# Optimization experiments

Measured on AMD Instinct MI355X. Metric: run time of the kernel, lower is better.

Reference implementation:

```python
import jax, jax.numpy as jnp
import numpy as np

B, C, H, W = 4, 64, 128, 128
D_INNER, D_STATE, DT_RANK, K = 192, 16, 6, 4  # d_model = 3*C//2 = 96, expand = 2
EPS = 1e-5


def _haar():
    # pywt db1: dec_lo=[s,s], dec_hi=[-s,s]; code reverses dec_* and uses rec_* in
    # original order -> for Haar both dec and rec filter banks are identical.
    s = np.float32(1.0 / np.sqrt(2.0))
    lo = np.array([s, s], np.float32)
    hi = np.array([s, -s], np.float32)
    # stack order: [lo(i)lo(j), hi(i)lo(j), lo(i)hi(j), hi(i)hi(j)]
    return np.stack([np.outer(lo, lo), np.outer(hi, lo),
                     np.outer(lo, hi), np.outer(hi, hi)], 0)  # (4,2,2)

DEC = jnp.asarray(_haar())
REC = jnp.asarray(_haar())
DN = ('NCHW', 'OIHW', 'NCHW')


def _ln(x, s, b):
    m = x.mean(-1, keepdims=True)
    v = x.var(-1, keepdims=True)
    return (x - m) * jax.lax.rsqrt(v + EPS) * s + b


def _wt(x):
    b, c, h, w = x.shape
    wf = jnp.tile(DEC[:, None], (c, 1, 1, 1))  # (4c,1,2,2), groups=c, pad=0 for db1
    y = jax.lax.conv_general_dilated(x, wf, (2, 2), 'VALID',
                                     feature_group_count=c, dimension_numbers=DN)
    return y.reshape(b, c, 4, h // 2, w // 2)


def _iwt(x):
    # conv_transpose2d(stride=2, pad=0, groups=c) == lhs-dilated conv with flipped kernel, pad k-1
    b, c = x.shape[0], x.shape[1]
    h2, w2 = x.shape[3], x.shape[4]
    xr = x.reshape(b, c * 4, h2, w2)
    wf = jnp.tile(REC[:, ::-1, ::-1][None], (c, 1, 1, 1))  # (c,4,2,2)
    return jax.lax.conv_general_dilated(xr, wf, (1, 1), ((1, 1), (1, 1)),
                                        lhs_dilation=(2, 2), feature_group_count=c,
                                        dimension_numbers=DN)


def _ss2d(x, in_proj_w, conv_dw_w, conv_dw_b, x_proj_w, dt_proj_w, dt_proj_b,
          A_log, Ds, out_norm_s, out_norm_b, out_proj_w):
    b, d, h, w = x.shape  # d == D_INNER
    L = h * w
    xz = jnp.einsum('bchw,ec->behw', x, in_proj_w)  # (b,2d,h,w)
    x1, z = xz[:, :d], xz[:, d:]
    x1 = jax.lax.conv_general_dilated(x1, conv_dw_w, (1, 1), ((1, 1), (1, 1)),
                                      feature_group_count=d, dimension_numbers=DN)
    x1 = jax.nn.silu(x1 + conv_dw_b[None, :, None, None])
    # 4-direction flattening: hw, wh, and their reverses
    xf = x1.reshape(b, d, L)
    xt = x1.transpose(0, 1, 3, 2).reshape(b, d, L)
    xs = jnp.stack([xf, xt], 1)
    xs = jnp.concatenate([xs, xs[..., ::-1]], 1)  # (b,K,d,L)
    x_dbl = jnp.einsum('bkdl,kcd->bkcl', xs, x_proj_w)
    dts = x_dbl[:, :, :DT_RANK]
    Bs = x_dbl[:, :, DT_RANK:DT_RANK + D_STATE]   # (b,K,n,L)
    Cs = x_dbl[:, :, DT_RANK + D_STATE:]
    delta = jax.nn.softplus(jnp.einsum('bkrl,kdr->bkdl', dts, dt_proj_w)
                            + dt_proj_b[None, :, :, None])
    A = -jnp.exp(A_log)  # (K,d,n)

    def step(hc, inp):
        d_t, u_t, b_t, c_t = inp  # (b,K,d),(b,K,d),(b,K,n),(b,K,n)
        dA = jnp.exp(d_t[..., None] * A[None])
        hc = hc * dA + (d_t * u_t)[..., None] * b_t[:, :, None, :]
        y = jnp.einsum('bkdn,bkn->bkd', hc, c_t)
        return hc, y

    h0 = jnp.zeros((b, K, d, D_STATE), x.dtype)
    inputs = (delta.transpose(3, 0, 1, 2), xs.transpose(3, 0, 1, 2),
              Bs.transpose(3, 0, 1, 2), Cs.transpose(3, 0, 1, 2))
    _, ys = jax.lax.scan(step, h0, inputs)            # (L,b,K,d)
    out_y = ys.transpose(1, 2, 3, 0) + xs * Ds[None, :, :, None]  # (b,K,d,L)
    inv_y = out_y[:, 2:][..., ::-1]
    wh = out_y[:, 1].reshape(b, d, w, h).transpose(0, 1, 3, 2).reshape(b, d, L)
    invwh = inv_y[:, 1].reshape(b, d, w, h).transpose(0, 1, 3, 2).reshape(b, d, L)
    y = out_y[:, 0] + inv_y[:, 0] + wh + invwh        # (b,d,L)
    y = _ln(y.reshape(b, d, h, w).transpose(0, 2, 3, 1), out_norm_s, out_norm_b)
    y = y * jax.nn.silu(z.transpose(0, 2, 3, 1))
    y = jnp.einsum('bhwd,ed->bhwe', y, out_proj_w)
    return y.transpose(0, 3, 1, 2)


def reference(x, wt_low_scale, wt_high_scale, low_conv_w, in_proj_w, conv_dw_w,
              conv_dw_b, x_proj_w, dt_proj_w, dt_proj_b, A_log, Ds,
              out_norm_s, out_norm_b, out_proj_w, ln2_s, ln2_b, eca_w):
    b, c = x.shape[0], x.shape[1]
    wt = _wt(x)                                       # (b,c,4,h2,w2)
    h2, w2 = wt.shape[3], wt.shape[4]
    low = wt[:, :, 0] * wt_low_scale
    high = wt[:, :, 1:].reshape(b, c * 3, h2, w2) * wt_high_scale
    low = jax.nn.silu(jnp.einsum('bchw,ec->behw', low, low_conv_w[:, :, 0, 0]))
    high = _ss2d(high, in_proj_w, conv_dw_w, conv_dw_b, x_proj_w, dt_proj_w,
                 dt_proj_b, A_log, Ds, out_norm_s, out_norm_b, out_proj_w)
    high = _ln(high.transpose(0, 2, 3, 1), ln2_s, ln2_b).transpose(0, 3, 1, 2)
    mamba = jnp.tile(low, (1, 3, 1, 1)) * high
    merged = jnp.concatenate([low, mamba], 1).reshape(b, c, 4, h2, w2)
    y = _iwt(merged)                                  # (b,c,h,w)
    # ECA: gap -> conv1d(k=5) over channels -> sigmoid gate
    pooled = y.mean((2, 3))[:, None, :]               # (b,1,c)
    att = jax.lax.conv_general_dilated(pooled, eca_w.reshape(1, 1, 5), (1,),
                                       ((2, 2),), dimension_numbers=('NCH', 'OIH', 'NCH'))
    att = jax.nn.sigmoid(att[:, 0])
    return y * att[:, :, None, None] + x


def setup_inputs():
    key = jax.random.key(0)
    ks = jax.random.split(key, 20)
    f = jax.random.normal
    return {
        'x': f(ks[0], (B, C, H, W), jnp.float32),
        'wt_low_scale': jax.random.uniform(ks[1], (1, C, 1, 1), jnp.float32),
        'wt_high_scale': jax.random.uniform(ks[2], (1, 3 * C, 1, 1), jnp.float32),
        'low_conv_w': f(ks[3], (C, C, 1, 1), jnp.float32) * 0.1,
        'in_proj_w': f(ks[4], (2 * D_INNER, D_INNER), jnp.float32) * 0.05,
        'conv_dw_w': f(ks[5], (D_INNER, 1, 3, 3), jnp.float32) * 0.3,
        'conv_dw_b': f(ks[6], (D_INNER,), jnp.float32) * 0.1,
        'x_proj_w': f(ks[7], (K, DT_RANK + 2 * D_STATE, D_INNER), jnp.float32) * 0.05,
        'dt_proj_w': f(ks[8], (K, D_INNER, DT_RANK), jnp.float32) * 0.1,
        'dt_proj_b': jax.random.uniform(ks[9], (K, D_INNER), jnp.float32) - 4.0,
        'A_log': jax.random.uniform(ks[10], (K, D_INNER, D_STATE), jnp.float32),
        'Ds': f(ks[11], (K, D_INNER), jnp.float32) * 0.1,
        'out_norm_s': jnp.ones((D_INNER,), jnp.float32),
        'out_norm_b': jnp.zeros((D_INNER,), jnp.float32),
        'out_proj_w': f(ks[12], (D_INNER, D_INNER), jnp.float32) * 0.05,
        'ln2_s': jnp.ones((3 * C,), jnp.float32),
        'ln2_b': jnp.zeros((3 * C,), jnp.float32),
        'eca_w': f(ks[13], (5,), jnp.float32) * 0.3,
    }
```

## Files before the change

kernel.cpp:

```cpp
#include <hip/hip_runtime.h>

constexpr int cB = 4, cC = 64, cH = 128, cW = 128;
constexpr int cL = 4096;
constexpr int cD = 192, cN = 16;
constexpr int NCH = 64, CHUNK = 64;

__device__ __forceinline__ float silu_f(float v) { return v / (1.f + __expf(-v)); }

__global__ __launch_bounds__(256) void k_wt(const float* __restrict__ x,
                                            const float* __restrict__ wls,
                                            const float* __restrict__ whs,
                                            float* __restrict__ lraw,
                                            float* __restrict__ high) {
    int idx = blockIdx.x * 256 + threadIdx.x;
    int j = idx & 63, i = (idx >> 6) & 63, c = (idx >> 12) & 63, b = idx >> 18;
    const float* xp = x + (((size_t)(b * cC + c)) * cH + 2 * i) * cW + 2 * j;
    float x00 = xp[0], x01 = xp[1], x10 = xp[cW], x11 = xp[cW + 1];
    float s0 = 0.5f * (x00 + x01 + x10 + x11);
    float s1 = 0.5f * (x00 + x01 - x10 - x11);
    float s2 = 0.5f * (x00 - x01 + x10 - x11);
    float s3 = 0.5f * (x00 - x01 - x10 + x11);
    int l = i * 64 + j;
    lraw[(size_t)(b * cC + c) * cL + l] = s0 * wls[c];
    int ch = c * 3;
    high[(size_t)(b * cD + ch + 0) * cL + l] = s1 * whs[ch + 0];
    high[(size_t)(b * cD + ch + 1) * cL + l] = s2 * whs[ch + 1];
    high[(size_t)(b * cD + ch + 2) * cL + l] = s3 * whs[ch + 2];
}

__global__ __launch_bounds__(256) void k_lowconv(const float* __restrict__ lraw,
                                                 const float* __restrict__ w,
                                                 float* __restrict__ lowT) {
    int bid = blockIdx.x;
    int lt0 = (bid & 63) * 64;
    int b = bid >> 6;
    __shared__ float sW[16][68];
    __shared__ float sI[16][68];
    int tid = threadIdx.x;
    int tl = tid & 15, te = tid >> 4;
    float acc[4][4];
#pragma unroll
    for (int i = 0; i < 4; i++)
#pragma unroll
        for (int j = 0; j < 4; j++) acc[i][j] = 0.f;
    for (int c0 = 0; c0 < 64; c0 += 16) {
#pragma unroll
        for (int q = 0; q < 4; q++) {
            int tt = tid + q * 256;
            int cc = tt & 15, ee = tt >> 4;
            sW[cc][ee] = w[ee * 64 + c0 + cc];
        }
#pragma unroll
        for (int q = 0; q < 4; q++) {
            int tt = tid + q * 256;
            int ll = tt & 63, cc = tt >> 6;
            sI[cc][ll] = lraw[(size_t)(b * cC + c0 + cc) * cL + lt0 + ll];
        }
        __syncthreads();
#pragma unroll
        for (int cc = 0; cc < 16; cc++) {
            float4 wv = *reinterpret_cast<const float4*>(&sW[cc][te * 4]);
            float4 iv = *reinterpret_cast<const float4*>(&sI[cc][tl * 4]);
            acc[0][0] = fmaf(wv.x, iv.x, acc[0][0]); acc[0][1] = fmaf(wv.x, iv.y, acc[0][1]);
            acc[0][2] = fmaf(wv.x, iv.z, acc[0][2]); acc[0][3] = fmaf(wv.x, iv.w, acc[0][3]);
            acc[1][0] = fmaf(wv.y, iv.x, acc[1][0]); acc[1][1] = fmaf(wv.y, iv.y, acc[1][1]);
            acc[1][2] = fmaf(wv.y, iv.z, acc[1][2]); acc[1][3] = fmaf(wv.y, iv.w, acc[1][3]);
            acc[2][0] = fmaf(wv.z, iv.x, acc[2][0]); acc[2][1] = fmaf(wv.z, iv.y, acc[2][1]);
            acc[2][2] = fmaf(wv.z, iv.z, acc[2][2]); acc[2][3] = fmaf(wv.z, iv.w, acc[2][3]);
            acc[3][0] = fmaf(wv.w, iv.x, acc[3][0]); acc[3][1] = fmaf(wv.w, iv.y, acc[3][1]);
            acc[3][2] = fmaf(wv.w, iv.z, acc[3][2]); acc[3][3] = fmaf(wv.w, iv.w, acc[3][3]);
        }
        __syncthreads();
    }
    int ebase = te * 4;
    int lbase = lt0 + tl * 4;
#pragma unroll
    for (int j = 0; j < 4; j++) {
        float4 v = make_float4(silu_f(acc[0][j]), silu_f(acc[1][j]), silu_f(acc[2][j]), silu_f(acc[3][j]));
        *reinterpret_cast<float4*>(&lowT[((size_t)b * cL + lbase + j) * 64 + ebase]) = v;
    }
}

__global__ __launch_bounds__(256) void k_inproj(const float* __restrict__ hi,
                                                const float* __restrict__ w,
                                                float* __restrict__ xout,
                                                float* __restrict__ zT) {
    int bid = blockIdx.x;
    int et = bid % 6;
    int blt = bid / 6;
    int lt0 = (blt & 63) * 64;
    int b = blt >> 6;
    int e0 = et * 64;
    __shared__ float sW[16][68];
    __shared__ float sI[16][68];
    int tid = threadIdx.x;
    int tl = tid & 15, te = tid >> 4;
    float acc[4][4];
#pragma unroll
    for (int i = 0; i < 4; i++)
#pragma unroll
        for (int j = 0; j < 4; j++) acc[i][j] = 0.f;
    for (int c0 = 0; c0 < 192; c0 += 16) {
#pragma unroll
        for (int q = 0; q < 4; q++) {
            int tt = tid + q * 256;
            int cc = tt & 15, ee = tt >> 4;
            sW[cc][ee] = w[(e0 + ee) * 192 + c0 + cc];
        }
#pragma unroll
        for (int q = 0; q < 4; q++) {
            int tt = tid + q * 256;
            int ll = tt & 63, cc = tt >> 6;
            sI[cc][ll] = hi[(size_t)(b * cD + c0 + cc) * cL + lt0 + ll];
        }
        __syncthreads();
#pragma unroll
        for (int cc = 0; cc < 16; cc++) {
            float4 wv = *reinterpret_cast<const float4*>(&sW[cc][te * 4]);
            float4 iv = *reinterpret_cast<const float4*>(&sI[cc][tl * 4]);
            acc[0][0] = fmaf(wv.x, iv.x, acc[0][0]); acc[0][1] = fmaf(wv.x, iv.y, acc[0][1]);
            acc[0][2] = fmaf(wv.x, iv.z, acc[0][2]); acc[0][3] = fmaf(wv.x, iv.w, acc[0][3]);
            acc[1][0] = fmaf(wv.y, iv.x, acc[1][0]); acc[1][1] = fmaf(wv.y, iv.y, acc[1][1]);
            acc[1][2] = fmaf(wv.y, iv.z, acc[1][2]); acc[1][3] = fmaf(wv.y, iv.w, acc[1][3]);
            acc[2][0] = fmaf(wv.z, iv.x, acc[2][0]); acc[2][1] = fmaf(wv.z, iv.y, acc[2][1]);
            acc[2][2] = fmaf(wv.z, iv.z, acc[2][2]); acc[2][3] = fmaf(wv.z, iv.w, acc[2][3]);
            acc[3][0] = fmaf(wv.w, iv.x, acc[3][0]); acc[3][1] = fmaf(wv.w, iv.y, acc[3][1]);
            acc[3][2] = fmaf(wv.w, iv.z, acc[3][2]); acc[3][3] = fmaf(wv.w, iv.w, acc[3][3]);
        }
        __syncthreads();
    }
    int ebase = e0 + te * 4;
    int lbase = lt0 + tl * 4;
    if (ebase < 192) {
#pragma unroll
        for (int i = 0; i < 4; i++) {
            *reinterpret_cast<float4*>(&xout[(size_t)(b * cD + ebase + i) * cL + lbase]) =
                make_float4(acc[i][0], acc[i][1], acc[i][2], acc[i][3]);
        }
    } else {
#pragma unroll
        for (int j = 0; j < 4; j++) {
            *reinterpret_cast<float4*>(&zT[((size_t)b * cL + lbase + j) * 192 + (ebase - 192)]) =
                make_float4(acc[0][j], acc[1][j], acc[2][j], acc[3][j]);
        }
    }
}

__global__ __launch_bounds__(256) void k_dwconv(const float* __restrict__ xin,
                                                const float* __restrict__ w,
                                                const float* __restrict__ bias,
                                                float* __restrict__ x1,
                                                float* __restrict__ u1) {
    int bd = blockIdx.x;
    int d = bd % cD;
    const float* xp = xin + (size_t)bd * cL;
    float wv[9];
#pragma unroll
    for (int t = 0; t < 9; t++) wv[t] = w[d * 9 + t];
    float bv = bias[d];
    __shared__ float sm[64][65];
    int tid = threadIdx.x;
#pragma unroll
    for (int q = 0; q < 16; q++) {
        int p = tid + q * 256;
        int i = p >> 6, j = p & 63;
        float acc = bv;
#pragma unroll
        for (int di = 0; di < 3; di++) {
            int ii = i + di - 1;
            if (ii < 0 || ii >= 64) continue;
#pragma unroll
            for (int dj = 0; dj < 3; dj++) {
                int jj = j + dj - 1;
                if (jj < 0 || jj >= 64) continue;
                acc = fmaf(wv[di * 3 + dj], xp[ii * 64 + jj], acc);
            }
        }
        sm[i][j] = silu_f(acc);
    }
    __syncthreads();
#pragma unroll
    for (int q = 0; q < 16; q++) {
        int p = tid + q * 256;
        x1[(size_t)bd * cL + p] = sm[p >> 6][p & 63];
        u1[(size_t)bd * cL + p] = sm[p & 63][p >> 6];
    }
}

__global__ __launch_bounds__(256) void k_xproj(const float* __restrict__ x1,
                                               const float* __restrict__ u1,
                                               const float* __restrict__ xpw,
                                               float* __restrict__ xdbl) {
    int bid = blockIdx.x;
    int lt0 = (bid & 63) * 64;
    int k = (bid >> 6) & 3;
    int b = bid >> 8;
    const float* src = (k & 1) ? u1 : x1;
    bool rev = (k >= 2);
    __shared__ float sW[16][68];
    __shared__ float sI[16][68];
    int tid = threadIdx.x;
    int tl = tid & 15, te = tid >> 4;
    float acc[4][4];
#pragma unroll
    for (int i = 0; i < 4; i++)
#pragma unroll
        for (int j = 0; j < 4; j++) acc[i][j] = 0.f;
    for (int c0 = 0; c0 < 192; c0 += 16) {
#pragma unroll
        for (int q = 0; q < 4; q++) {
            int tt = tid + q * 256;
            int cc = tt & 15, ee = tt >> 4;
            sW[cc][ee] = (ee < 38) ? xpw[(k * 38 + ee) * 192 + c0 + cc] : 0.f;
        }
#pragma unroll
        for (int q = 0; q < 4; q++) {
            int tt = tid + q * 256;
            int ll = tt & 63, cc = tt >> 6;
            int l = lt0 + ll;
            int lm = rev ? (cL - 1 - l) : l;
            sI[cc][ll] = src[(size_t)(b * cD + c0 + cc) * cL + lm];
        }
        __syncthreads();
#pragma unroll
        for (int cc = 0; cc < 16; cc++) {
            float4 wv = *reinterpret_cast<const float4*>(&sW[cc][te * 4]);
            float4 iv = *reinterpret_cast<const float4*>(&sI[cc][tl * 4]);
            acc[0][0] = fmaf(wv.x, iv.x, acc[0][0]); acc[0][1] = fmaf(wv.x, iv.y, acc[0][1]);
            acc[0][2] = fmaf(wv.x, iv.z, acc[0][2]); acc[0][3] = fmaf(wv.x, iv.w, acc[0][3]);
            acc[1][0] = fmaf(wv.y, iv.x, acc[1][0]); acc[1][1] = fmaf(wv.y, iv.y, acc[1][1]);
            acc[1][2] = fmaf(wv.y, iv.z, acc[1][2]); acc[1][3] = fmaf(wv.y, iv.w, acc[1][3]);
            acc[2][0] = fmaf(wv.z, iv.x, acc[2][0]); acc[2][1] = fmaf(wv.z, iv.y, acc[2][1]);
            acc[2][2] = fmaf(wv.z, iv.z, acc[2][2]); acc[2][3] = fmaf(wv.z, iv.w, acc[2][3]);
            acc[3][0] = fmaf(wv.w, iv.x, acc[3][0]); acc[3][1] = fmaf(wv.w, iv.y, acc[3][1]);
            acc[3][2] = fmaf(wv.w, iv.z, acc[3][2]); acc[3][3] = fmaf(wv.w, iv.w, acc[3][3]);
        }
        __syncthreads();
    }
    int lbase = lt0 + tl * 4;
#pragma unroll
    for (int i = 0; i < 4; i++) {
        int e = te * 4 + i;
        if (e < 38) {
            *reinterpret_cast<float4*>(&xdbl[(size_t)((b * 4 + k) * 38 + e) * cL + lbase]) =
                make_float4(acc[i][0], acc[i][1], acc[i][2], acc[i][3]);
        }
    }
}

__global__ __launch_bounds__(192) void k_scan1(const float* __restrict__ xdbl,
                                               const float* __restrict__ x1,
                                               const float* __restrict__ u1,
                                               const float* __restrict__ dtw,
                                               const float* __restrict__ dtb,
                                               const float* __restrict__ alog,
                                               float* __restrict__ P,
                                               float* __restrict__ S) {
    int bid = blockIdx.x;
    int ch = bid % NCH;
    int bk = bid / NCH;
    int k = bk & 3, b = bk >> 2;
    int tid = threadIdx.x;
    int d = tid;
    float Av2[16], h[16];
#pragma unroll
    for (int j = 0; j < 16; j++) {
        Av2[j] = -__expf(alog[(k * 192 + d) * 16 + j]) * 1.44269504088896f;
        h[j] = 0.f;
    }
    float dtbv = dtb[k * 192 + d];
    float dtwv[6];
#pragma unroll
    for (int r = 0; r < 6; r++) dtwv[r] = dtw[(k * 192 + d) * 6 + r];
    const float* dtrows = xdbl + (size_t)(bk * 38) * cL;
    const float* Brow = xdbl + (size_t)(bk * 38 + 6) * cL;
    const float* ubase = ((k & 1) ? u1 : x1) + ((size_t)b * cD + d) * cL;
    bool rev = (k >= 2);

    __shared__ float sB[2][16][16];
    __shared__ float sdt[2][16][8];

    int rowA = tid >> 4, colA = tid & 15;
    int p0 = ch * CHUNK;

    for (int idx = tid; idx < 256; idx += 192)
        sB[0][idx & 15][idx >> 4] = Brow[(size_t)(idx >> 4) * cL + p0 + (idx & 15)];
    if (tid < 96) sdt[0][colA][rowA] = dtrows[(size_t)rowA * cL + p0 + colA];

    float Q = 0.f;
    int cur = 0;
    for (int t0 = p0; t0 < p0 + CHUNK; t0 += 16) {
        __syncthreads();
        if (t0 + 16 < p0 + CHUNK) {
            int t1 = t0 + 16;
            for (int idx = tid; idx < 256; idx += 192)
                sB[cur ^ 1][idx & 15][idx >> 4] = Brow[(size_t)(idx >> 4) * cL + t1 + (idx & 15)];
            if (tid < 96) sdt[cur ^ 1][colA][rowA] = dtrows[(size_t)rowA * cL + t1 + colA];
        }
        float uvals[16];
        {
            const float* up = rev ? (ubase + (cL - 16 - t0)) : (ubase + t0);
#pragma unroll
            for (int q = 0; q < 4; q++)
                *reinterpret_cast<float4*>(&uvals[q * 4]) = *reinterpret_cast<const float4*>(up + q * 4);
        }
#pragma unroll
        for (int l = 0; l < 16; l++) {
            float acc = dtbv;
#pragma unroll
            for (int r = 0; r < 6; r++) acc = fmaf(dtwv[r], sdt[cur][l][r], acc);
            float sp = fmaxf(acc, 0.f) + __logf(1.f + __expf(-fabsf(acc)));
            Q += sp;
            float uv = rev ? uvals[15 - l] : uvals[l];
            float duB = sp * uv;
            float Bv[16];
            *reinterpret_cast<float4*>(&Bv[0])  = *reinterpret_cast<const float4*>(&sB[cur][l][0]);
            *reinterpret_cast<float4*>(&Bv[4])  = *reinterpret_cast<const float4*>(&sB[cur][l][4]);
            *reinterpret_cast<float4*>(&Bv[8])  = *reinterpret_cast<const float4*>(&sB[cur][l][8]);
            *reinterpret_cast<float4*>(&Bv[12]) = *reinterpret_cast<const float4*>(&sB[cur][l][12]);
#pragma unroll
            for (int j = 0; j < 16; j++)
                h[j] = fmaf(h[j], exp2f(sp * Av2[j]), duB * Bv[j]);
        }
        cur ^= 1;
    }
    size_t base = (size_t)bid * 16 * 192 + d;
#pragma unroll
    for (int j = 0; j < 16; j++) {
        P[base + (size_t)j * 192] = exp2f(Av2[j] * Q);
        S[base + (size_t)j * 192] = h[j];
    }
}

__global__ __launch_bounds__(256) void k_carry(const float* __restrict__ P,
                                               float* __restrict__ S) {
    int gid = blockIdx.x * 256 + threadIdx.x;
    int d = gid % 192;
    int n = (gid / 192) & 15;
    int bk = gid / 3072;
    float h = 0.f;
    for (int c = 0; c < NCH; c++) {
        size_t idx = ((size_t)(bk * NCH + c) * 16 + n) * 192 + d;
        h = fmaf(P[idx], h, S[idx]);
        S[idx] = h;
    }
}

__global__ __launch_bounds__(192) void k_scan2(const float* __restrict__ xdbl,
                                               const float* __restrict__ x1,
                                               const float* __restrict__ u1,
                                               const float* __restrict__ dtw,
                                               const float* __restrict__ dtb,
                                               const float* __restrict__ alog,
                                               const float* __restrict__ dss,
                                               const float* __restrict__ S,
                                               float* __restrict__ yacc) {
    int bid = blockIdx.x;
    int ch = bid % NCH;
    int bk = bid / NCH;
    int k = bk & 3, b = bk >> 2;
    int tid = threadIdx.x;
    int d = tid;
    float Av2[16], h[16];
#pragma unroll
    for (int j = 0; j < 16; j++) {
        Av2[j] = -__expf(alog[(k * 192 + d) * 16 + j]) * 1.44269504088896f;
        h[j] = (ch == 0) ? 0.f : S[((size_t)(bk * NCH + ch - 1) * 16 + j) * 192 + d];
    }
    float Dv = dss[k * 192 + d];
    float dtbv = dtb[k * 192 + d];
    float dtwv[6];
#pragma unroll
    for (int r = 0; r < 6; r++) dtwv[r] = dtw[(k * 192 + d) * 6 + r];
    const float* dtrows = xdbl + (size_t)(bk * 38) * cL;
    const float* Brow = xdbl + (size_t)(bk * 38 + 6) * cL;
    const float* Crow = xdbl + (size_t)(bk * 38 + 22) * cL;
    const float* ubase = ((k & 1) ? u1 : x1) + ((size_t)b * cD + d) * cL;
    bool rev = (k >= 2);

    __shared__ float sB[2][16][16];
    __shared__ float sC[2][16][16];
    __shared__ float sdt[2][16][8];

    int rowA = tid >> 4, colA = tid & 15;
    int p0 = ch * CHUNK;

    for (int idx = tid; idx < 256; idx += 192) {
        sB[0][idx & 15][idx >> 4] = Brow[(size_t)(idx >> 4) * cL + p0 + (idx & 15)];
        sC[0][idx & 15][idx >> 4] = Crow[(size_t)(idx >> 4) * cL + p0 + (idx & 15)];
    }
    if (tid < 96) sdt[0][colA][rowA] = dtrows[(size_t)rowA * cL + p0 + colA];

    int cur = 0;
    for (int t0 = p0; t0 < p0 + CHUNK; t0 += 16) {
        __syncthreads();
        if (t0 + 16 < p0 + CHUNK) {
            int t1 = t0 + 16;
            for (int idx = tid; idx < 256; idx += 192) {
                sB[cur ^ 1][idx & 15][idx >> 4] = Brow[(size_t)(idx >> 4) * cL + t1 + (idx & 15)];
                sC[cur ^ 1][idx & 15][idx >> 4] = Crow[(size_t)(idx >> 4) * cL + t1 + (idx & 15)];
            }
            if (tid < 96) sdt[cur ^ 1][colA][rowA] = dtrows[(size_t)rowA * cL + t1 + colA];
        }
        float uvals[16];
        {
            const float* up = rev ? (ubase + (cL - 16 - t0)) : (ubase + t0);
#pragma unroll
            for (int q = 0; q < 4; q++)
                *reinterpret_cast<float4*>(&uvals[q * 4]) = *reinterpret_cast<const float4*>(up + q * 4);
        }
#pragma unroll
        for (int l = 0; l < 16; l++) {
            float acc = dtbv;
#pragma unroll
            for (int r = 0; r < 6; r++) acc = fmaf(dtwv[r], sdt[cur][l][r], acc);
            float sp = fmaxf(acc, 0.f) + __logf(1.f + __expf(-fabsf(acc)));
            float uv = rev ? uvals[15 - l] : uvals[l];
            float duB = sp * uv;
            float Bv[16], Cv[16];
            *reinterpret_cast<float4*>(&Bv[0])  = *reinterpret_cast<const float4*>(&sB[cur][l][0]);
            *reinterpret_cast<float4*>(&Bv[4])  = *reinterpret_cast<const float4*>(&sB[cur][l][4]);
            *reinterpret_cast<float4*>(&Bv[8])  = *reinterpret_cast<const float4*>(&sB[cur][l][8]);
            *reinterpret_cast<float4*>(&Bv[12]) = *reinterpret_cast<const float4*>(&sB[cur][l][12]);
            *reinterpret_cast<float4*>(&Cv[0])  = *reinterpret_cast<const float4*>(&sC[cur][l][0]);
            *reinterpret_cast<float4*>(&Cv[4])  = *reinterpret_cast<const float4*>(&sC[cur][l][4]);
            *reinterpret_cast<float4*>(&Cv[8])  = *reinterpret_cast<const float4*>(&sC[cur][l][8]);
            *reinterpret_cast<float4*>(&Cv[12]) = *reinterpret_cast<const float4*>(&sC[cur][l][12]);
            float yA = 0.f, yB = 0.f;
#pragma unroll
            for (int j = 0; j < 8; j++) {
                h[j] = fmaf(h[j], exp2f(sp * Av2[j]), duB * Bv[j]);
                yA = fmaf(h[j], Cv[j], yA);
            }
#pragma unroll
            for (int j = 8; j < 16; j++) {
                h[j] = fmaf(h[j], exp2f(sp * Av2[j]), duB * Bv[j]);
                yB = fmaf(h[j], Cv[j], yB);
            }
            float y = yA + yB + uv * Dv;
            int lg = t0 + l;
            int lm;
            if (k == 0) lm = lg;
            else if (k == 1) lm = (lg & 63) * 64 + (lg >> 6);
            else if (k == 2) lm = cL - 1 - lg;
            else { int qq = cL - 1 - lg; lm = (qq & 63) * 64 + (qq >> 6); }
            atomicAdd(&yacc[((size_t)b * cL + lm) * 192 + d], y);
        }
        cur ^= 1;
    }
}

__global__ __launch_bounds__(256) void k_comb(const float* __restrict__ yacc,
                                              const float* __restrict__ zT,
                                              const float* __restrict__ ons,
                                              const float* __restrict__ onb,
                                              float* __restrict__ yln) {
    int bid = blockIdx.x;
    int b = bid >> 10;
    int pg = bid & 1023;
    int tid = threadIdx.x;
    int wq = tid >> 6, lane = tid & 63;
    int l = pg * 4 + wq;
    float v[3];
    float s = 0.f, s2 = 0.f;
#pragma unroll
    for (int m = 0; m < 3; m++) {
        int d = lane + 64 * m;
        float t = yacc[((size_t)b * cL + l) * 192 + d];
        v[m] = t;
        s += t;
        s2 += t * t;
    }
#pragma unroll
    for (int o = 1; o < 64; o <<= 1) {
        s += __shfl_xor(s, o);
        s2 += __shfl_xor(s2, o);
    }
    float mean = s / 192.f;
    float var = s2 / 192.f - mean * mean;
    float rstd = rsqrtf(var + 1e-5f);
#pragma unroll
    for (int m = 0; m < 3; m++) {
        int d = lane + 64 * m;
        float zv = zT[((size_t)b * cL + l) * 192 + d];
        float yn = (v[m] - mean) * rstd * ons[d] + onb[d];
        yln[((size_t)b * cL + l) * 192 + d] = yn * silu_f(zv);
    }
}

__global__ __launch_bounds__(256) void k_outproj(const float* __restrict__ yln,
                                                 const float* __restrict__ w,
                                                 float* __restrict__ hout) {
    int bid = blockIdx.x;
    int lt0 = (bid & 63) * 64;
    int et = (bid >> 6) % 3;
    int b = bid / 192;
    int e0 = et * 64;
    __shared__ float sW[16][68];
    __shared__ float sI[16][68];
    int tid = threadIdx.x;
    int tl = tid & 15, te = tid >> 4;
    float acc[4][4];
#pragma unroll
    for (int i = 0; i < 4; i++)
#pragma unroll
        for (int j = 0; j < 4; j++) acc[i][j] = 0.f;
    for (int c0 = 0; c0 < 192; c0 += 16) {
#pragma unroll
        for (int q = 0; q < 4; q++) {
            int tt = tid + q * 256;
            int cc = tt & 15, ee = tt >> 4;
            sW[cc][ee] = w[(e0 + ee) * 192 + c0 + cc];
        }
#pragma unroll
        for (int q = 0; q < 4; q++) {
            int tt = tid + q * 256;
            int cc = tt & 15, lq = tt >> 4;
            sI[cc][lq] = yln[((size_t)b * cL + lt0 + lq) * 192 + c0 + cc];
        }
        __syncthreads();
#pragma unroll
        for (int cc = 0; cc < 16; cc++) {
            float4 wv = *reinterpret_cast<const float4*>(&sW[cc][te * 4]);
            float4 iv = *reinterpret_cast<const float4*>(&sI[cc][tl * 4]);
            acc[0][0] = fmaf(wv.x, iv.x, acc[0][0]); acc[0][1] = fmaf(wv.x, iv.y, acc[0][1]);
            acc[0][2] = fmaf(wv.x, iv.z, acc[0][2]); acc[0][3] = fmaf(wv.x, iv.w, acc[0][3]);
            acc[1][0] = fmaf(wv.y, iv.x, acc[1][0]); acc[1][1] = fmaf(wv.y, iv.y, acc[1][1]);
            acc[1][2] = fmaf(wv.y, iv.z, acc[1][2]); acc[1][3] = fmaf(wv.y, iv.w, acc[1][3]);
            acc[2][0] = fmaf(wv.z, iv.x, acc[2][0]); acc[2][1] = fmaf(wv.z, iv.y, acc[2][1]);
            acc[2][2] = fmaf(wv.z, iv.z, acc[2][2]); acc[2][3] = fmaf(wv.z, iv.w, acc[2][3]);
            acc[3][0] = fmaf(wv.w, iv.x, acc[3][0]); acc[3][1] = fmaf(wv.w, iv.y, acc[3][1]);
            acc[3][2] = fmaf(wv.w, iv.z, acc[3][2]); acc[3][3] = fmaf(wv.w, iv.w, acc[3][3]);
        }
        __syncthreads();
    }
    int ebase = e0 + te * 4;
    int lbase = lt0 + tl * 4;
#pragma unroll
    for (int j = 0; j < 4; j++) {
        *reinterpret_cast<float4*>(&hout[((size_t)b * cL + lbase + j) * 192 + ebase]) =
            make_float4(acc[0][j], acc[1][j], acc[2][j], acc[3][j]);
    }
}

__global__ __launch_bounds__(256) void k_ln2(const float* __restrict__ hout,
                                             const float* __restrict__ lowT,
                                             const float* __restrict__ l2s,
                                             const float* __restrict__ l2b,
                                             float* __restrict__ merged) {
    int bid = blockIdx.x;
    int b = bid >> 10;
    int pg = bid & 1023;
    int tid = threadIdx.x;
    int wq = tid >> 6, lane = tid & 63;
    int l = pg * 4 + wq;
    float v[3];
    float s = 0.f, s2 = 0.f;
#pragma unroll
    for (int m = 0; m < 3; m++) {
        int d = lane + 64 * m;
        float t = hout[((size_t)b * cL + l) * 192 + d];
        v[m] = t;
        s += t;
        s2 += t * t;
    }
#pragma unroll
    for (int o = 1; o < 64; o <<= 1) {
        s += __shfl_xor(s, o);
        s2 += __shfl_xor(s2, o);
    }
    float mean = s / 192.f;
    float var = s2 / 192.f - mean * mean;
    float rstd = rsqrtf(var + 1e-5f);
    float lv = lowT[((size_t)b * cL + l) * 64 + lane];
    float* mp = merged + ((size_t)b * cL + l) * 256;
    mp[lane] = lv;
#pragma unroll
    for (int m = 0; m < 3; m++) {
        int d = lane + 64 * m;
        float hn = (v[m] - mean) * rstd * l2s[d] + l2b[d];
        mp[64 + d] = lv * hn;
    }
}

__global__ __launch_bounds__(256) void k_iwt(const float* __restrict__ merged,
                                             float* __restrict__ ypre) {
    int idx = blockIdx.x * 256 + threadIdx.x;
    int j = idx & 63, i = (idx >> 6) & 63, g = (idx >> 12) & 63, b = idx >> 18;
    const float4 mv = *reinterpret_cast<const float4*>(merged + ((size_t)b * cL + i * 64 + j) * 256 + g * 4);
    float m0 = mv.x, m1 = mv.y, m2 = mv.z, m3 = mv.w;
    float* yp = ypre + ((size_t)(b * 64 + g) * cH + 2 * i) * cW + 2 * j;
    float2 r0 = make_float2(0.5f * (m0 + m1 + m2 + m3), 0.5f * (m0 + m1 - m2 - m3));
    float2 r1 = make_float2(0.5f * (m0 - m1 + m2 - m3), 0.5f * (m0 - m1 - m2 + m3));
    *reinterpret_cast<float2*>(yp) = r0;
    *reinterpret_cast<float2*>(yp + cW) = r1;
}

__global__ __launch_bounds__(256) void k_pool(const float* __restrict__ ypre,
                                              float* __restrict__ pooled) {
    int bg = blockIdx.x;
    const float* p = ypre + (size_t)bg * (cH * cW);
    float s = 0.f;
    for (int t = threadIdx.x; t < cH * cW; t += 256) s += p[t];
#pragma unroll
    for (int o = 1; o < 64; o <<= 1) s += __shfl_xor(s, o);
    __shared__ float red[4];
    if ((threadIdx.x & 63) == 0) red[threadIdx.x >> 6] = s;
    __syncthreads();
    if (threadIdx.x == 0) pooled[bg] = (red[0] + red[1] + red[2] + red[3]) * (1.f / (cH * cW));
}

__global__ __launch_bounds__(256) void k_eca(const float* __restrict__ pooled,
                                             const float* __restrict__ w,
                                             float* __restrict__ att) {
    int t = threadIdx.x;
    int b = t >> 6, c = t & 63;
    float s = 0.f;
#pragma unroll
    for (int u = 0; u < 5; u++) {
        int cc = c + u - 2;
        if (cc >= 0 && cc < 64) s += w[u] * pooled[b * 64 + cc];
    }
    att[t] = 1.f / (1.f + __expf(-s));
}

__global__ __launch_bounds__(256) void k_final(const float* __restrict__ ypre,
                                               const float* __restrict__ x,
                                               const float* __restrict__ att,
                                               float* __restrict__ out) {
    int idx = blockIdx.x * 256 + threadIdx.x;
    size_t base = (size_t)idx * 4;
    int bc = (int)(base >> 14);
    float a = att[bc];
    float4 yv = *reinterpret_cast<const float4*>(ypre + base);
    float4 xv = *reinterpret_cast<const float4*>(x + base);
    float4 o;
    o.x = fmaf(yv.x, a, xv.x);
    o.y = fmaf(yv.y, a, xv.y);
    o.z = fmaf(yv.z, a, xv.z);
    o.w = fmaf(yv.w, a, xv.w);
    *reinterpret_cast<float4*>(out + base) = o;
}

extern "C" void kernel_launch(void* const* d_in, const int* in_sizes, int n_in,
                              void* d_out, int out_size, void* d_ws, size_t ws_size,
                              hipStream_t stream) {
    const float* x    = (const float*)d_in[0];
    const float* wls  = (const float*)d_in[1];
    const float* whs  = (const float*)d_in[2];
    const float* lcw  = (const float*)d_in[3];
    const float* ipw  = (const float*)d_in[4];
    const float* dww  = (const float*)d_in[5];
    const float* dwb  = (const float*)d_in[6];
    const float* xpw  = (const float*)d_in[7];
    const float* dtw  = (const float*)d_in[8];
    const float* dtb  = (const float*)d_in[9];
    const float* alog = (const float*)d_in[10];
    const float* dss  = (const float*)d_in[11];
    const float* ons  = (const float*)d_in[12];
    const float* onb  = (const float*)d_in[13];
    const float* opw  = (const float*)d_in[14];
    const float* l2s  = (const float*)d_in[15];
    const float* l2b  = (const float*)d_in[16];
    const float* ecw  = (const float*)d_in[17];
    float* out = (float*)d_out;
    float* w = (float*)d_ws;

    float* high   = w + 0;
    float* lraw   = w + 3145728;
    float* lowT   = w + 4194304;
    float* xbuf   = w + 5242880;
    float* zT     = w + 8388608;
    float* x1     = w + 11534336;
    float* u1     = w + 14680064;
    float* yacc   = w + 17825792;
    float* Sbuf   = w + 20971520;
    float* xdbl   = high;
    float* Pbuf   = xbuf;
    float* yln    = xbuf;
    float* hout   = high;
    float* merged = x1;
    float* ypre   = yacc;
    float* pooled = lraw;
    float* att    = lraw + 256;

    k_wt<<<4096, 256, 0, stream>>>(x, wls, whs, lraw, high);
    k_lowconv<<<256, 256, 0, stream>>>(lraw, lcw, lowT);
    k_inproj<<<1536, 256, 0, stream>>>(high, ipw, xbuf, zT);
    k_dwconv<<<768, 256, 0, stream>>>(xbuf, dww, dwb, x1, u1);
    k_xproj<<<1024, 256, 0, stream>>>(x1, u1, xpw, xdbl);
    hipMemsetAsync(yacc, 0, (size_t)cB * cL * cD * sizeof(float), stream);
    k_scan1<<<1024, 192, 0, stream>>>(xdbl, x1, u1, dtw, dtb, alog, Pbuf, Sbuf);
    k_carry<<<192, 256, 0, stream>>>(Pbuf, Sbuf);
    k_scan2<<<1024, 192, 0, stream>>>(xdbl, x1, u1, dtw, dtb, alog, dss, Sbuf, yacc);
    k_comb<<<4096, 256, 0, stream>>>(yacc, zT, ons, onb, yln);
    k_outproj<<<768, 256, 0, stream>>>(yln, opw, hout);
    k_ln2<<<4096, 256, 0, stream>>>(hout, lowT, l2s, l2b, merged);
    k_iwt<<<4096, 256, 0, stream>>>(merged, ypre);
    k_pool<<<256, 256, 0, stream>>>(ypre, pooled);
    k_eca<<<1, 256, 0, stream>>>(pooled, ecw, att);
    k_final<<<4096, 256, 0, stream>>>(ypre, x, att, out);
}
```

Baseline: 374.9 us.

## Register-prefetch scan tiles, pass chunk dt sums to carry, fuse pooling into IWT

The scan kernels now load the next 16-step tile of B, C, dt and u into registers before the current tile's recurrence and write them to shared memory afterwards, so global latency overlaps with compute. The loop is fully unrolled. scan1 stores only the per-chunk dt sum Q instead of 16 decay products per channel, and the carry kernel recomputes exp2(A*Q), which cuts intermediate memory traffic. The average pool is folded into k_iwt through wave reductions and atomics, removing one kernel and a full re-read of ypre. This adds a memset, float atomic ordering nondeterminism, and higher register pressure in the scans.

```diff
diff --git a/kernel.cpp b/kernel.cpp
--- a/kernel.cpp
+++ b/kernel.cpp
@@ -254,7 +254,7 @@
                                                const float* __restrict__ dtw,
                                                const float* __restrict__ dtb,
                                                const float* __restrict__ alog,
-                                               float* __restrict__ P,
+                                               float* __restrict__ Qb,
                                                float* __restrict__ S) {
     int bid = blockIdx.x;
     int ch = bid % NCH;
@@ -280,29 +280,35 @@
     __shared__ float sB[2][16][16];
     __shared__ float sdt[2][16][8];
 
-    int rowA = tid >> 4, colA = tid & 15;
     int p0 = ch * CHUNK;
-
-    for (int idx = tid; idx < 256; idx += 192)
-        sB[0][idx & 15][idx >> 4] = Brow[(size_t)(idx >> 4) * cL + p0 + (idx & 15)];
-    if (tid < 96) sdt[0][colA][rowA] = dtrows[(size_t)rowA * cL + p0 + colA];
-
+    int e1 = tid + 192;
+
+    sB[0][tid & 15][tid >> 4] = Brow[(size_t)(tid >> 4) * cL + p0 + (tid & 15)];
+    if (e1 < 256) sB[0][e1 & 15][e1 >> 4] = Brow[(size_t)(e1 >> 4) * cL + p0 + (e1 & 15)];
+    if (tid < 96) sdt[0][tid & 15][tid >> 4] = dtrows[(size_t)(tid >> 4) * cL + p0 + (tid & 15)];
+    float uu[2][16];
+    {
+        const float* up = rev ? (ubase + (cL - 16 - p0)) : (ubase + p0);
+#pragma unroll
+        for (int q = 0; q < 4; q++)
+            *reinterpret_cast<float4*>(&uu[0][q * 4]) = *reinterpret_cast<const float4*>(up + q * 4);
+    }
     float Q = 0.f;
-    int cur = 0;
-    for (int t0 = p0; t0 < p0 + CHUNK; t0 += 16) {
-        __syncthreads();
-        if (t0 + 16 < p0 + CHUNK) {
-            int t1 = t0 + 16;
-            for (int idx = tid; idx < 256; idx += 192)
-                sB[cur ^ 1][idx & 15][idx >> 4] = Brow[(size_t)(idx >> 4) * cL + t1 + (idx & 15)];
-            if (tid < 96) sdt[cur ^ 1][colA][rowA] = dtrows[(size_t)rowA * cL + t1 + colA];
-        }
-        float uvals[16];
-        {
-            const float* up = rev ? (ubase + (cL - 16 - t0)) : (ubase + t0);
+#pragma unroll
+    for (int it = 0; it < CHUNK / 16; it++) {
+        const int cur = it & 1;
+        __syncthreads();
+        float rb0 = 0.f, rb1 = 0.f, rdt = 0.f;
+        const bool hasNext = (it + 1 < CHUNK / 16);
+        if (hasNext) {
+            int t1 = p0 + it * 16 + 16;
+            rb0 = Brow[(size_t)(tid >> 4) * cL + t1 + (tid & 15)];
+            if (e1 < 256) rb1 = Brow[(size_t)(e1 >> 4) * cL + t1 + (e1 & 15)];
+            if (tid < 96) rdt = dtrows[(size_t)(tid >> 4) * cL + t1 + (tid & 15)];
+            const float* up = rev ? (ubase + (cL - 16 - t1)) : (ubase + t1);
 #pragma unroll
             for (int q = 0; q < 4; q++)
-                *reinterpret_cast<float4*>(&uvals[q * 4]) = *reinterpret_cast<const float4*>(up + q * 4);
+                *reinterpret_cast<float4*>(&uu[cur ^ 1][q * 4]) = *reinterpret_cast<const float4*>(up + q * 4);
         }
 #pragma unroll
         for (int l = 0; l < 16; l++) {
@@ -311,7 +317,7 @@
             for (int r = 0; r < 6; r++) acc = fmaf(dtwv[r], sdt[cur][l][r], acc);
             float sp = fmaxf(acc, 0.f) + __logf(1.f + __expf(-fabsf(acc)));
             Q += sp;
-            float uv = rev ? uvals[15 - l] : uvals[l];
+            float uv = rev ? uu[cur][15 - l] : uu[cur][l];
             float duB = sp * uv;
             float Bv[16];
             *reinterpret_cast<float4*>(&Bv[0])  = *reinterpret_cast<const float4*>(&sB[cur][l][0]);
@@ -322,26 +328,32 @@
             for (int j = 0; j < 16; j++)
                 h[j] = fmaf(h[j], exp2f(sp * Av2[j]), duB * Bv[j]);
         }
-        cur ^= 1;
+        if (hasNext) {
+            sB[cur ^ 1][tid & 15][tid >> 4] = rb0;
+            if (e1 < 256) sB[cur ^ 1][e1 & 15][e1 >> 4] = rb1;
+            if (tid < 96) sdt[cur ^ 1][tid & 15][tid >> 4] = rdt;
+        }
     }
     size_t base = (size_t)bid * 16 * 192 + d;
 #pragma unroll
-    for (int j = 0; j < 16; j++) {
-        P[base + (size_t)j * 192] = exp2f(Av2[j] * Q);
-        S[base + (size_t)j * 192] = h[j];
-    }
-}
-
-__global__ __launch_bounds__(256) void k_carry(const float* __restrict__ P,
-                                               float* __restrict__ S) {
+    for (int j = 0; j < 16; j++) S[base + (size_t)j * 192] = h[j];
+    Qb[(size_t)bid * 192 + d] = Q;
+}
+
+__global__ __launch_bounds__(256) void k_carryQ(const float* __restrict__ alog,
+                                                const float* __restrict__ Qb,
+                                                float* __restrict__ S) {
     int gid = blockIdx.x * 256 + threadIdx.x;
     int d = gid % 192;
     int n = (gid / 192) & 15;
     int bk = gid / 3072;
+    int k = bk & 3;
+    float Av2 = -__expf(alog[(k * 192 + d) * 16 + n]) * 1.44269504088896f;
     float h = 0.f;
     for (int c = 0; c < NCH; c++) {
+        size_t qidx = (size_t)(bk * NCH + c) * 192 + d;
         size_t idx = ((size_t)(bk * NCH + c) * 16 + n) * 192 + d;
-        h = fmaf(P[idx], h, S[idx]);
+        h = fmaf(exp2f(Av2 * Qb[qidx]), h, S[idx]);
         S[idx] = h;
     }
 }
@@ -382,32 +394,43 @@
     __shared__ float sC[2][16][16];
     __shared__ float sdt[2][16][8];
 
-    int rowA = tid >> 4, colA = tid & 15;
     int p0 = ch * CHUNK;
-
-    for (int idx = tid; idx < 256; idx += 192) {
-        sB[0][idx & 15][idx >> 4] = Brow[(size_t)(idx >> 4) * cL + p0 + (idx & 15)];
-        sC[0][idx & 15][idx >> 4] = Crow[(size_t)(idx >> 4) * cL + p0 + (idx & 15)];
-    }
-    if (tid < 96) sdt[0][colA][rowA] = dtrows[(size_t)rowA * cL + p0 + colA];
-
-    int cur = 0;
-    for (int t0 = p0; t0 < p0 + CHUNK; t0 += 16) {
-        __syncthreads();
-        if (t0 + 16 < p0 + CHUNK) {
+    int e1 = tid + 192;
+
+    sB[0][tid & 15][tid >> 4] = Brow[(size_t)(tid >> 4) * cL + p0 + (tid & 15)];
+    sC[0][tid & 15][tid >> 4] = Crow[(size_t)(tid >> 4) * cL + p0 + (tid & 15)];
+    if (e1 < 256) {
+        sB[0][e1 & 15][e1 >> 4] = Brow[(size_t)(e1 >> 4) * cL + p0 + (e1 & 15)];
+        sC[0][e1 & 15][e1 >> 4] = Crow[(size_t)(e1 >> 4) * cL + p0 + (e1 & 15)];
+    }
+    if (tid < 96) sdt[0][tid & 15][tid >> 4] = dtrows[(size_t)(tid >> 4) * cL + p0 + (tid & 15)];
+    float uu[2][16];
+    {
+        const float* up = rev ? (ubase + (cL - 16 - p0)) : (ubase + p0);
+#pragma unroll
+        for (int q = 0; q < 4; q++)
+            *reinterpret_cast<float4*>(&uu[0][q * 4]) = *reinterpret_cast<const float4*>(up + q * 4);
+    }
+#pragma unroll
+    for (int it = 0; it < CHUNK / 16; it++) {
+        const int cur = it & 1;
+        int t0 = p0 + it * 16;
+        __syncthreads();
+        float rb0 = 0.f, rb1 = 0.f, rc0 = 0.f, rc1 = 0.f, rdt = 0.f;
+        const bool hasNext = (it + 1 < CHUNK / 16);
+        if (hasNext) {
             int t1 = t0 + 16;
-            for (int idx = tid; idx < 256; idx += 192) {
-                sB[cur ^ 1][idx & 15][idx >> 4] = Brow[(size_t)(idx >> 4) * cL + t1 + (idx & 15)];
-                sC[cur ^ 1][idx & 15][idx >> 4] = Crow[(size_t)(idx >> 4) * cL + t1 + (idx & 15)];
+            rb0 = Brow[(size_t)(tid >> 4) * cL + t1 + (tid & 15)];
+            rc0 = Crow[(size_t)(tid >> 4) * cL + t1 + (tid & 15)];
+            if (e1 < 256) {
+                rb1 = Brow[(size_t)(e1 >> 4) * cL + t1 + (e1 & 15)];
+                rc1 = Crow[(size_t)(e1 >> 4) * cL + t1 + (e1 & 15)];
             }
-            if (tid < 96) sdt[cur ^ 1][colA][rowA] = dtrows[(size_t)rowA * cL + t1 + colA];
-        }
-        float uvals[16];
-        {
-            const float* up = rev ? (ubase + (cL - 16 - t0)) : (ubase + t0);
+            if (tid < 96) rdt = dtrows[(size_t)(tid >> 4) * cL + t1 + (tid & 15)];
+            const float* up = rev ? (ubase + (cL - 16 - t1)) : (ubase + t1);
 #pragma unroll
             for (int q = 0; q < 4; q++)
-                *reinterpret_cast<float4*>(&uvals[q * 4]) = *reinterpret_cast<const float4*>(up + q * 4);
+                *reinterpret_cast<float4*>(&uu[cur ^ 1][q * 4]) = *reinterpret_cast<const float4*>(up + q * 4);
         }
 #pragma unroll
         for (int l = 0; l < 16; l++) {
@@ -415,7 +438,7 @@
 #pragma unroll
             for (int r = 0; r < 6; r++) acc = fmaf(dtwv[r], sdt[cur][l][r], acc);
             float sp = fmaxf(acc, 0.f) + __logf(1.f + __expf(-fabsf(acc)));
-            float uv = rev ? uvals[15 - l] : uvals[l];
+            float uv = rev ? uu[cur][15 - l] : uu[cur][l];
             float duB = sp * uv;
             float Bv[16], Cv[16];
             *reinterpret_cast<float4*>(&Bv[0])  = *reinterpret_cast<const float4*>(&sB[cur][l][0]);
@@ -446,7 +469,15 @@
             else { int qq = cL - 1 - lg; lm = (qq & 63) * 64 + (qq >> 6); }
             atomicAdd(&yacc[((size_t)b * cL + lm) * 192 + d], y);
         }
-        cur ^= 1;
+        if (hasNext) {
+            sB[cur ^ 1][tid & 15][tid >> 4] = rb0;
+            sC[cur ^ 1][tid & 15][tid >> 4] = rc0;
+            if (e1 < 256) {
+                sB[cur ^ 1][e1 & 15][e1 >> 4] = rb1;
+                sC[cur ^ 1][e1 & 15][e1 >> 4] = rc1;
+            }
+            if (tid < 96) sdt[cur ^ 1][tid & 15][tid >> 4] = rdt;
+        }
     }
 }
 
@@ -584,7 +615,8 @@
 }
 
 __global__ __launch_bounds__(256) void k_iwt(const float* __restrict__ merged,
-                                             float* __restrict__ ypre) {
+                                             float* __restrict__ ypre,
+                                             float* __restrict__ pooled) {
     int idx = blockIdx.x * 256 + threadIdx.x;
     int j = idx & 63, i = (idx >> 6) & 63, g = (idx >> 12) & 63, b = idx >> 18;
     const float4 mv = *reinterpret_cast<const float4*>(merged + ((size_t)b * cL + i * 64 + j) * 256 + g * 4);
@@ -594,20 +626,10 @@
     float2 r1 = make_float2(0.5f * (m0 - m1 + m2 - m3), 0.5f * (m0 - m1 - m2 + m3));
     *reinterpret_cast<float2*>(yp) = r0;
     *reinterpret_cast<float2*>(yp + cW) = r1;
-}
-
-__global__ __launch_bounds__(256) void k_pool(const float* __restrict__ ypre,
-                                              float* __restrict__ pooled) {
-    int bg = blockIdx.x;
-    const float* p = ypre + (size_t)bg * (cH * cW);
-    float s = 0.f;
-    for (int t = threadIdx.x; t < cH * cW; t += 256) s += p[t];
-#pragma unroll
-    for (int o = 1; o < 64; o <<= 1) s += __shfl_xor(s, o);
-    __shared__ float red[4];
-    if ((threadIdx.x & 63) == 0) red[threadIdx.x >> 6] = s;
-    __syncthreads();
-    if (threadIdx.x == 0) pooled[bg] = (red[0] + red[1] + red[2] + red[3]) * (1.f / (cH * cW));
+    float ssum = r0.x + r0.y + r1.x + r1.y;
+#pragma unroll
+    for (int o = 1; o < 64; o <<= 1) ssum += __shfl_xor(ssum, o);
+    if ((threadIdx.x & 63) == 0) atomicAdd(&pooled[b * 64 + g], ssum * (1.f / (cH * cW)));
 }
 
 __global__ __launch_bounds__(256) void k_eca(const float* __restrict__ pooled,
@@ -675,8 +697,8 @@
     float* u1     = w + 14680064;
     float* yacc   = w + 17825792;
     float* Sbuf   = w + 20971520;
+    float* Qbuf   = w + 24117248;
     float* xdbl   = high;
-    float* Pbuf   = xbuf;
     float* yln    = xbuf;
     float* hout   = high;
     float* merged = x1;
@@ -690,14 +712,14 @@
     k_dwconv<<<768, 256, 0, stream>>>(xbuf, dww, dwb, x1, u1);
     k_xproj<<<1024, 256, 0, stream>>>(x1, u1, xpw, xdbl);
     hipMemsetAsync(yacc, 0, (size_t)cB * cL * cD * sizeof(float), stream);
-    k_scan1<<<1024, 192, 0, stream>>>(xdbl, x1, u1, dtw, dtb, alog, Pbuf, Sbuf);
-    k_carry<<<192, 256, 0, stream>>>(Pbuf, Sbuf);
+    hipMemsetAsync(pooled, 0, 256 * sizeof(float), stream);
+    k_scan1<<<1024, 192, 0, stream>>>(xdbl, x1, u1, dtw, dtb, alog, Qbuf, Sbuf);
+    k_carryQ<<<192, 256, 0, stream>>>(alog, Qbuf, Sbuf);
     k_scan2<<<1024, 192, 0, stream>>>(xdbl, x1, u1, dtw, dtb, alog, dss, Sbuf, yacc);
     k_comb<<<4096, 256, 0, stream>>>(yacc, zT, ons, onb, yln);
     k_outproj<<<768, 256, 0, stream>>>(yln, opw, hout);
     k_ln2<<<4096, 256, 0, stream>>>(hout, lowT, l2s, l2b, merged);
-    k_iwt<<<4096, 256, 0, stream>>>(merged, ypre);
-    k_pool<<<256, 256, 0, stream>>>(ypre, pooled);
+    k_iwt<<<4096, 256, 0, stream>>>(merged, ypre, pooled);
     k_eca<<<1, 256, 0, stream>>>(pooled, ecw, att);
     k_final<<<4096, 256, 0, stream>>>(ypre, x, att, out);
 }
```

New measurement: 1.090 ms. +190.9%, slower.
